# Kernel tuning notes

Hardware: AMD Instinct MI355X
Metric: run time of the kernel (lower is better)

Reference implementation:

```python
import jax, jax.numpy as jnp
import numpy as np

EPS = 1e-5      # InstanceNorm2d default eps
SLOPE = 0.2     # leaky relu negative_slope
K = 16          # neighbors
C = 128         # feature_dim


def _knn_idx(coords, k):
    # coords: [B,3,N] -> idx [B,N,k] of k nearest neighbors (excluding self)
    x = jnp.transpose(coords, (0, 2, 1))            # [B,N,3]
    sq = jnp.sum(x * x, axis=-1)                    # [B,N]
    dist = sq[:, :, None] + sq[:, None, :] - 2.0 * jnp.einsum('bnd,bmd->bnm', x, x)
    _, idx = jax.lax.top_k(-dist, k + 1)            # smallest distances, sorted
    return idx[:, :, 1:]                            # drop self


def _graph_feature(feats, idx):
    # feats: [B,C,N], idx: [B,N,k] -> [B,2C,N,k] = cat(center, neighbor-center)
    neigh = jax.vmap(lambda f, i: f[:, i])(feats, idx)   # [B,C,N,k]
    center = feats[:, :, :, None]
    return jnp.concatenate(
        [jnp.broadcast_to(center, neigh.shape), neigh - center], axis=1)


def _inorm(x):
    # InstanceNorm2d (affine=False): normalize each (b,c) over spatial dims
    mean = jnp.mean(x, axis=(2, 3), keepdims=True)
    var = jnp.mean((x - mean) ** 2, axis=(2, 3), keepdims=True)
    return (x - mean) * jax.lax.rsqrt(var + EPS)


def _edge_block(x, W):
    # 1x1 conv (W: [O,I]) + instance norm + leaky relu, x: [B,I,N,k]
    h = jnp.einsum('oi,bink->bonk', W, x)
    return jax.nn.leaky_relu(_inorm(h), SLOPE)


def setup_inputs() -> dict:
    key = jax.random.key(0)
    k1, k2, k3, k4, k5 = jax.random.split(key, 5)
    B, N = 2, 8192
    coords = jax.random.normal(k1, (B, 3, N), dtype=jnp.float32)
    features = jax.random.normal(k2, (B, C, N), dtype=jnp.float32)
    W1 = jax.random.normal(k3, (C, 2 * C), dtype=jnp.float32) * 0.05
    W2 = jax.random.normal(k4, (2 * C, 2 * C), dtype=jnp.float32) * 0.05
    W3 = jax.random.normal(k5, (C, 4 * C), dtype=jnp.float32) * 0.05
    return {"coords": coords, "features": features, "W1": W1, "W2": W2, "W3": W3}


def reference(coords, features, W1, W2, W3):
    idx = _knn_idx(coords, K)                       # [B,N,K]
    x0 = features                                   # [B,C,N]
    # block 1: EdgeConv C -> C
    x1 = _edge_block(_graph_feature(x0, idx), W1)   # [B,C,N,K]
    x1 = jnp.max(x1, axis=-1)                       # [B,C,N]
    # block 2: EdgeConv C -> 2C (same coords => same knn indices)
    x2 = _edge_block(_graph_feature(x1, idx), W2)   # [B,2C,N,K]
    x2 = jnp.max(x2, axis=-1)                       # [B,2C,N]
    # fuse: 1x1 conv 4C -> C + instance norm (over N) + leaky relu
    x3 = jnp.concatenate([x0, x1, x2], axis=1)      # [B,4C,N]
    h = jnp.einsum('oi,bin->bon', W3, x3)           # [B,C,N]
    h = _inorm(h[:, :, :, None])[:, :, :, 0]
    return jax.nn.leaky_relu(h, SLOPE)
```

## Files before the change

kernel.cpp:

```cpp
#include <hip/hip_runtime.h>
#include <hip/hip_bf16.h>
#include <cstdint>
#include <cstddef>

#define B_ 2
#define N_ 8192
#define C_ 128
#define K_ 16
#define NK_ (N_ * K_)
#define EPS_ 1e-5f
#define SLOPE_ 0.2f
#define INF_ 3.0e38f

typedef __attribute__((ext_vector_type(8))) short short8;
typedef __attribute__((ext_vector_type(4))) float f32x4;

static constexpr size_t OFF_IDX   = 0x000000;
static constexpr size_t OFF_CPK   = 0x100000;
static constexpr size_t OFF_CPK64 = 0x140000;
static constexpr size_t OFF_ACC   = 0x1C0000;
static constexpr size_t OFF_WC1   = 0x1D0000;
static constexpr size_t OFF_WC2   = 0x1E0000;
static constexpr size_t OFF_WB3   = 0x200000;
static constexpr size_t OFF_X3T   = 0x240000;
static constexpr size_t OFF_PQ    = OFF_X3T + (size_t)B_ * N_ * 512 * 2;

__device__ __forceinline__ __hip_bfloat16 ftob(float f) { return __float2bfloat16(f); }

__global__ void prep_kernel(const float* __restrict__ coords,
                            const float* __restrict__ W1,
                            const float* __restrict__ W2,
                            const float* __restrict__ W3,
                            __hip_bfloat16* __restrict__ wc1, __hip_bfloat16* __restrict__ wc2,
                            __hip_bfloat16* __restrict__ wb3,
                            float4* __restrict__ cpk, double4* __restrict__ cpk64,
                            float* __restrict__ acc) {
  int tid = blockIdx.x * 256 + threadIdx.x;
  if (tid < 32768) {
    int o = tid >> 7, i = tid & 127;
    float v;
    if (o < 128) v = W1[o * 256 + i] - W1[o * 256 + 128 + i];
    else         v = W1[(o - 128) * 256 + 128 + i];
    wc1[tid] = ftob(v);
  } else if (tid < 32768 + 65536) {
    int t2 = tid - 32768;
    int o = t2 >> 7, i = t2 & 127;
    float v;
    if (o < 256) v = W2[o * 256 + i] - W2[o * 256 + 128 + i];
    else         v = W2[(o - 256) * 256 + 128 + i];
    wc2[t2] = ftob(v);
  } else if (tid < 98304 + 65536) {
    int t2 = tid - 98304;
    wb3[t2] = ftob(W3[t2]);
  } else if (tid < 163840 + B_ * N_) {
    int q = tid - 163840;
    int b = q >> 13, n = q & (N_ - 1);
    float x = coords[(b * 3 + 0) * N_ + n];
    float y = coords[(b * 3 + 1) * N_ + n];
    float z = coords[(b * 3 + 2) * N_ + n];
    float sq = __fadd_rn(__fadd_rn(__fmul_rn(x, x), __fmul_rn(y, y)), __fmul_rn(z, z));
    cpk[q] = make_float4(x, y, z, sq);
    double xd = (double)x, yd = (double)y, zd = (double)z;
    double sqd = (xd * xd + yd * yd) + zd * zd;
    cpk64[q] = make_double4(xd, yd, zd, sqd);
  } else if (tid < 180224 + 2048) {
    acc[tid - 180224] = 0.f;
  }
}

__global__ __launch_bounds__(256) void transpose_kernel(const float* __restrict__ x0,
                                                        __hip_bfloat16* __restrict__ x3t) {
  __shared__ float tile[64 * 68];
  int b = blockIdx.z, c0 = blockIdx.y * 64, n0 = blockIdx.x * 64;
  int t = threadIdx.x;
  int r = t >> 4;
  int c4 = (t & 15) * 4;
#pragma unroll
  for (int i = 0; i < 4; ++i) {
    int row = r + i * 16;
    float4 v = *(const float4*)&x0[((size_t)(b * C_ + c0 + row)) * N_ + n0 + c4];
    *(float4*)&tile[row * 68 + c4] = v;
  }
  __syncthreads();
#pragma unroll
  for (int i = 0; i < 4; ++i) {
    int nl = r + i * 16;
    __hip_bfloat16* dst = &x3t[((size_t)(b * N_ + n0 + nl)) * 512 + c0 + c4];
    dst[0] = ftob(tile[(c4 + 0) * 68 + nl]);
    dst[1] = ftob(tile[(c4 + 1) * 68 + nl]);
    dst[2] = ftob(tile[(c4 + 2) * 68 + nl]);
    dst[3] = ftob(tile[(c4 + 3) * 68 + nl]);
  }
}

__device__ __forceinline__ float thresh17(float v, int lane) {
#pragma unroll
  for (int k2 = 2; k2 <= 64; k2 <<= 1) {
#pragma unroll
    for (int j = k2 >> 1; j > 0; j >>= 1) {
      float o = __shfl_xor(v, j, 64);
      bool up = ((lane & k2) == 0);
      bool lower = ((lane & j) == 0);
      v = ((lower == up)) ? fminf(v, o) : fmaxf(v, o);
    }
  }
  return __shfl(v, 16, 64);
}

__device__ __forceinline__ void bsort64d(double& d, int& ix, int lane) {
#pragma unroll
  for (int k2 = 2; k2 <= 64; k2 <<= 1) {
#pragma unroll
    for (int j = k2 >> 1; j > 0; j >>= 1) {
      double od = __shfl_xor(d, j, 64);
      int oi = __shfl_xor(ix, j, 64);
      bool up = ((lane & k2) == 0);
      bool lower = ((lane & j) == 0);
      bool takeMin = (lower == up);
      bool less = (od < d) || (od == d && oi < ix);
      if (takeMin == less) { d = od; ix = oi; }
    }
  }
}

__global__ __launch_bounds__(256) void knn_kernel(const float4* __restrict__ cpk,
                                                  const double4* __restrict__ cpk64,
                                                  int* __restrict__ idxout) {
  __shared__ int scnt[4][4];
  __shared__ int sii[4][4][128];
  int lane = threadIdx.x & 63;
  int wv = threadIdx.x >> 6;
  int q0 = (blockIdx.x * 4 + wv) * 4;
  int b = q0 >> 13;
  const float4* cb = cpk + (size_t)b * N_;
  const double4* cb64 = cpk64 + (size_t)b * N_;
  float4 me0 = cpk[q0], me1 = cpk[q0 + 1], me2 = cpk[q0 + 2], me3 = cpk[q0 + 3];

  if (lane < 4) scnt[wv][lane] = 0;
  __syncthreads();

  float m0 = INF_, m1 = INF_, m2 = INF_, m3 = INF_;
  for (int i = 0; i < 128; ++i) {
    float4 c = cb[i * 64 + lane];
    float d0 = fmaf(me0.z, c.z, fmaf(me0.y, c.y, me0.x * c.x));
    float d1 = fmaf(me1.z, c.z, fmaf(me1.y, c.y, me1.x * c.x));
    float d2 = fmaf(me2.z, c.z, fmaf(me2.y, c.y, me2.x * c.x));
    float d3 = fmaf(me3.z, c.z, fmaf(me3.y, c.y, me3.x * c.x));
    m0 = fminf(m0, fmaf(-2.0f, d0, c.w));
    m1 = fminf(m1, fmaf(-2.0f, d1, c.w));
    m2 = fminf(m2, fmaf(-2.0f, d2, c.w));
    m3 = fminf(m3, fmaf(-2.0f, d3, c.w));
  }
  float T0 = thresh17(m0, lane) + 1e-3f;
  float T1 = thresh17(m1, lane) + 1e-3f;
  float T2 = thresh17(m2, lane) + 1e-3f;
  float T3 = thresh17(m3, lane) + 1e-3f;

  for (int i = 0; i < 128; ++i) {
    float4 c = cb[i * 64 + lane];
    float d0 = fmaf(me0.z, c.z, fmaf(me0.y, c.y, me0.x * c.x));
    float d1 = fmaf(me1.z, c.z, fmaf(me1.y, c.y, me1.x * c.x));
    float d2 = fmaf(me2.z, c.z, fmaf(me2.y, c.y, me2.x * c.x));
    float d3 = fmaf(me3.z, c.z, fmaf(me3.y, c.y, me3.x * c.x));
    int m = i * 64 + lane;
    if (fmaf(-2.0f, d0, c.w) <= T0) { int p = atomicAdd(&scnt[wv][0], 1); if (p < 128) sii[wv][0][p] = m; }
    if (fmaf(-2.0f, d1, c.w) <= T1) { int p = atomicAdd(&scnt[wv][1], 1); if (p < 128) sii[wv][1][p] = m; }
    if (fmaf(-2.0f, d2, c.w) <= T2) { int p = atomicAdd(&scnt[wv][2], 1); if (p < 128) sii[wv][2][p] = m; }
    if (fmaf(-2.0f, d3, c.w) <= T3) { int p = atomicAdd(&scnt[wv][3], 1); if (p < 128) sii[wv][3][p] = m; }
  }
  __syncthreads();

#pragma unroll 1
  for (int j = 0; j < 4; ++j) {
    int q = q0 + j;
    int n = q & (N_ - 1);
    int cnt = scnt[wv][j] < 128 ? scnt[wv][j] : 128;
    double4 me64 = cb64[n];
    double d1 = 1e300; int ix1 = 0x7FFFFFFF;
    if (lane < cnt) {
      int m = sii[wv][j][lane];
      if (m != n) {
        double4 c = cb64[m];
        double dot = (me64.x * c.x + me64.y * c.y) + me64.z * c.z;
        d1 = (me64.w + c.w) - 2.0 * dot;
        ix1 = m;
      }
    }
    bsort64d(d1, ix1, lane);
    if (cnt > 64) {
      double d2 = 1e300; int ix2 = 0x7FFFFFFF;
      if (lane + 64 < cnt) {
        int m = sii[wv][j][lane + 64];
        if (m != n) {
          double4 c = cb64[m];
          double dot = (me64.x * c.x + me64.y * c.y) + me64.z * c.z;
          d2 = (me64.w + c.w) - 2.0 * dot;
          ix2 = m;
        }
      }
      bsort64d(d2, ix2, lane);
      int src = (lane - 16) & 63;
      double dB = __shfl(d2, src, 64);
      int iB = __shfl(ix2, src, 64);
      double nd = (lane < 16) ? d1 : ((lane < 32) ? dB : 1e300);
      int nix = (lane < 16) ? ix1 : ((lane < 32) ? iB : 0x7FFFFFFF);
      bsort64d(nd, nix, lane);
      d1 = nd; ix1 = nix;
    }
    if (lane < 16) idxout[(size_t)q * 16 + lane] = ix1;
  }
}

__global__ __launch_bounds__(256) void gemm_mfma(const __hip_bfloat16* __restrict__ X, int ldx,
                                                 const __hip_bfloat16* __restrict__ W, int ldw,
                                                 float* __restrict__ Cc, int ldc, int Ktot) {
  __shared__ short As[64 * 40];
  int b = blockIdx.z;
  int n0 = blockIdx.x * 64, o0 = blockIdx.y * 64;
  int t = threadIdx.x;
  int lane = t & 63, wv = t >> 6;
  int nh = (wv & 1) * 32, oh = (wv >> 1) * 32;
  const __hip_bfloat16* Xb = X + (size_t)(b * N_ + n0) * ldx;
  f32x4 acc00 = {0.f, 0.f, 0.f, 0.f}, acc01 = acc00, acc10 = acc00, acc11 = acc00;
  int sr = t >> 2;
  int sc = (t & 3) * 8;
  int arow = lane & 15;
  int kq = (lane >> 4) * 8;
  for (int kt = 0; kt < Ktot; kt += 32) {
    short8 av = *(const short8*)&Xb[(size_t)sr * ldx + kt + sc];
    *(short8*)&As[sr * 40 + sc] = av;
    __syncthreads();
    short8 a0 = *(const short8*)&As[(nh + arow) * 40 + kq];
    short8 a1 = *(const short8*)&As[(nh + 16 + arow) * 40 + kq];
    const __hip_bfloat16* Wp = W + (size_t)(o0 + oh + arow) * ldw + kt + kq;
    short8 b0 = *(const short8*)&Wp[0];
    short8 b1 = *(const short8*)&Wp[16 * (size_t)ldw];
    acc00 = __builtin_amdgcn_mfma_f32_16x16x32_bf16(a0, b0, acc00, 0, 0, 0);
    acc01 = __builtin_amdgcn_mfma_f32_16x16x32_bf16(a0, b1, acc01, 0, 0, 0);
    acc10 = __builtin_amdgcn_mfma_f32_16x16x32_bf16(a1, b0, acc10, 0, 0, 0);
    acc11 = __builtin_amdgcn_mfma_f32_16x16x32_bf16(a1, b1, acc11, 0, 0, 0);
    __syncthreads();
  }
  int crow = (lane >> 4) * 4;
  int ccol = lane & 15;
#pragma unroll
  for (int r = 0; r < 4; ++r) {
    size_t row0 = (size_t)(b * N_ + n0 + nh + crow + r) * ldc + o0 + oh;
    size_t row1 = (size_t)(b * N_ + n0 + nh + 16 + crow + r) * ldc + o0 + oh;
    Cc[row0 + ccol]      = acc00[r];
    Cc[row0 + 16 + ccol] = acc01[r];
    Cc[row1 + ccol]      = acc10[r];
    Cc[row1 + 16 + ccol] = acc11[r];
  }
}

template <int CO>
__global__ __launch_bounds__(256) void edge_kernel(const float* __restrict__ PQ,
                                                   const int* __restrict__ idx,
                                                   __hip_bfloat16* __restrict__ Mout,
                                                   float* __restrict__ acc) {
  constexpr int NG = 256 / CO;
  __shared__ float r1[256], r2[256];
  int b = blockIdx.y;
  int n0 = blockIdx.x * 64;
  int t = threadIdx.x;
  int o = t & (CO - 1);
  int qg = t / CO;
  float s1 = 0.f, s2 = 0.f;
  const float* PQb = PQ + (size_t)b * N_ * (2 * CO);
  for (int qq = qg; qq < 64; qq += NG) {
    int n = n0 + qq;
    const int4* ip = (const int4*)&idx[(size_t)(b * N_ + n) * 16];
    int4 i0 = ip[0], i1 = ip[1], i2 = ip[2], i3 = ip[3];
    float p = PQb[(size_t)n * (2 * CO) + o];
    float hmax = -INF_;
#define EDGE_STEP(mm)                                                    \
    { int mc = (mm) & (N_ - 1);                                          \
      float vv = PQb[(size_t)mc * (2 * CO) + CO + o];                    \
      float h = p + vv;                                                  \
      hmax = fmaxf(hmax, h); s1 += h; s2 = fmaf(h, h, s2); }
    EDGE_STEP(i0.x) EDGE_STEP(i0.y) EDGE_STEP(i0.z) EDGE_STEP(i0.w)
    EDGE_STEP(i1.x) EDGE_STEP(i1.y) EDGE_STEP(i1.z) EDGE_STEP(i1.w)
    EDGE_STEP(i2.x) EDGE_STEP(i2.y) EDGE_STEP(i2.z) EDGE_STEP(i2.w)
    EDGE_STEP(i3.x) EDGE_STEP(i3.y) EDGE_STEP(i3.z) EDGE_STEP(i3.w)
#undef EDGE_STEP
    Mout[(size_t)(b * N_ + n) * 512 + o] = ftob(hmax);
  }
  r1[t] = s1; r2[t] = s2;
  __syncthreads();
  if (t < CO) {
#pragma unroll
    for (int g = 1; g < NG; ++g) { s1 += r1[t + g * CO]; s2 += r2[t + g * CO]; }
    atomicAdd(&acc[(b * CO + o) * 2 + 0], s1);
    atomicAdd(&acc[(b * CO + o) * 2 + 1], s2);
  }
}

template <int CO>
__global__ void norm_kernel(__hip_bfloat16* __restrict__ M, const float* __restrict__ acc) {
  int tid = blockIdx.x * 256 + threadIdx.x;
  int o = tid & (CO - 1);
  int bn = tid / CO;
  int b = bn >> 13;
  float s1 = acc[(b * CO + o) * 2], s2 = acc[(b * CO + o) * 2 + 1];
  const float inv = 1.f / (float)NK_;
  float mean = s1 * inv;
  float var = fmaf(s2, inv, -mean * mean);
  float rs = rsqrtf(var + EPS_);
  float v = __bfloat162float(M[(size_t)bn * 512 + o]);
  float y = (v - mean) * rs;
  M[(size_t)bn * 512 + o] = ftob(y > 0.f ? y : SLOPE_ * y);
}

__global__ __launch_bounds__(256) void colred_kernel(const float* __restrict__ H,
                                                     float* __restrict__ acc3) {
  __shared__ float r1[256], r2[256];
  int b = blockIdx.y;
  int n0 = blockIdx.x * 256;
  int t = threadIdx.x;
  int o = t & 127, half = t >> 7;
  float s1 = 0.f, s2 = 0.f;
  for (int i = 0; i < 128; ++i) {
    int n = n0 + half * 128 + i;
    float v = H[(size_t)(b * N_ + n) * 128 + o];
    s1 += v; s2 = fmaf(v, v, s2);
  }
  r1[t] = s1; r2[t] = s2;
  __syncthreads();
  if (t < 128) {
    s1 = r1[t] + r1[t + 128];
    s2 = r2[t] + r2[t + 128];
    atomicAdd(&acc3[(b * 128 + o) * 2 + 0], s1);
    atomicAdd(&acc3[(b * 128 + o) * 2 + 1], s2);
  }
}

__global__ __launch_bounds__(256) void final_kernel(const float* __restrict__ H,
                                                    const float* __restrict__ acc3,
                                                    float* __restrict__ out) {
  __shared__ float tile[64 * 132];
  int b = blockIdx.y, n0 = blockIdx.x * 64;
  int t = threadIdx.x;
  int r = t >> 5;
  int c4 = (t & 31) * 4;
#pragma unroll
  for (int i = 0; i < 8; ++i) {
    int row = r + i * 8;
    *(float4*)&tile[row * 132 + c4] = *(const float4*)&H[(size_t)(b * N_ + n0 + row) * 128 + c4];
  }
  __syncthreads();
  int o = t >> 1;
  int nh = (t & 1) * 32;
  float s1 = acc3[(b * 128 + o) * 2], s2 = acc3[(b * 128 + o) * 2 + 1];
  const float inv = 1.f / (float)N_;
  float mean = s1 * inv;
  float var = fmaf(s2, inv, -mean * mean);
  float rs = rsqrtf(var + EPS_);
#pragma unroll
  for (int i = 0; i < 32; ++i) {
    int nl = nh + i;
    float v = tile[nl * 132 + o];
    float y = (v - mean) * rs;
    y = y > 0.f ? y : SLOPE_ * y;
    out[(size_t)(b * 128 + o) * N_ + n0 + nl] = y;
  }
}

extern "C" void kernel_launch(void* const* d_in, const int* in_sizes, int n_in,
                              void* d_out, int out_size, void* d_ws, size_t ws_size,
                              hipStream_t stream) {
  const float* coords = (const float*)d_in[0];
  const float* feats = (const float*)d_in[1];
  const float* W1 = (const float*)d_in[2];
  const float* W2 = (const float*)d_in[3];
  const float* W3 = (const float*)d_in[4];
  char* ws = (char*)d_ws;
  int* idx = (int*)(ws + OFF_IDX);
  float4* cpk = (float4*)(ws + OFF_CPK);
  double4* cpk64 = (double4*)(ws + OFF_CPK64);
  float* acc = (float*)(ws + OFF_ACC);
  __hip_bfloat16* wc1 = (__hip_bfloat16*)(ws + OFF_WC1);
  __hip_bfloat16* wc2 = (__hip_bfloat16*)(ws + OFF_WC2);
  __hip_bfloat16* wb3 = (__hip_bfloat16*)(ws + OFF_WB3);
  __hip_bfloat16* x3t = (__hip_bfloat16*)(ws + OFF_X3T);
  float* pq = (float*)(ws + OFF_PQ);

  prep_kernel<<<712, 256, 0, stream>>>(coords, W1, W2, W3, wc1, wc2, wb3, cpk, cpk64, acc);
  transpose_kernel<<<dim3(128, 2, 2), 256, 0, stream>>>(feats, x3t);
  knn_kernel<<<1024, 256, 0, stream>>>(cpk, cpk64, idx);
  gemm_mfma<<<dim3(128, 4, 2), 256, 0, stream>>>(x3t, 512, wc1, 128, pq, 256, 128);
  edge_kernel<128><<<dim3(128, 2), 256, 0, stream>>>(pq, idx, x3t + 128, acc + 0);
  norm_kernel<128><<<(B_ * N_ * 128) / 256, 256, 0, stream>>>(x3t + 128, acc + 0);
  gemm_mfma<<<dim3(128, 8, 2), 256, 0, stream>>>(x3t + 128, 512, wc2, 128, pq, 512, 128);
  edge_kernel<256><<<dim3(128, 2), 256, 0, stream>>>(pq, idx, x3t + 256, acc + 512);
  norm_kernel<256><<<(B_ * N_ * 256) / 256, 256, 0, stream>>>(x3t + 256, acc + 512);
  gemm_mfma<<<dim3(128, 2, 2), 256, 0, stream>>>(x3t, 512, wb3, 512, pq, 128, 512);
  colred_kernel<<<dim3(32, 2), 256, 0, stream>>>(pq, acc + 1536);
  final_kernel<<<dim3(128, 2), 256, 0, stream>>>(pq, acc + 1536, (float*)d_out);
}
```

Baseline: 226.8 us.

## Store edge-conv GEMM outputs in bf16 and process two channels per thread

The P/Q projection GEMMs for the two EdgeConv blocks now write bf16 instead of fp32. The edge gather kernel reads packed bf16 pairs, so each thread handles two channels with 32-bit loads, roughly halving gather traffic. The knn kernel also folds the -2 factor into precomputed coefficients and skips the atomic-insert path when no query hits. Rounding P and Q to bf16 adds error to the pre-norm activations and the instance-norm statistics.

After: 211.2 us. 6.9% less time.

```diff
diff --git a/kernel.cpp b/kernel.cpp
--- a/kernel.cpp
+++ b/kernel.cpp
@@ -26,6 +26,10 @@
 static constexpr size_t OFF_PQ    = OFF_X3T + (size_t)B_ * N_ * 512 * 2;
 
 __device__ __forceinline__ __hip_bfloat16 ftob(float f) { return __float2bfloat16(f); }
+__device__ __forceinline__ float bf2f(unsigned short h) {
+  unsigned u = ((unsigned)h) << 16;
+  return __uint_as_float(u);
+}
 
 __global__ void prep_kernel(const float* __restrict__ coords,
                             const float* __restrict__ W1,
@@ -135,6 +139,10 @@
   const float4* cb = cpk + (size_t)b * N_;
   const double4* cb64 = cpk64 + (size_t)b * N_;
   float4 me0 = cpk[q0], me1 = cpk[q0 + 1], me2 = cpk[q0 + 2], me3 = cpk[q0 + 3];
+  float a0x = -2.f * me0.x, a0y = -2.f * me0.y, a0z = -2.f * me0.z;
+  float a1x = -2.f * me1.x, a1y = -2.f * me1.y, a1z = -2.f * me1.z;
+  float a2x = -2.f * me2.x, a2y = -2.f * me2.y, a2z = -2.f * me2.z;
+  float a3x = -2.f * me3.x, a3y = -2.f * me3.y, a3z = -2.f * me3.z;
 
   if (lane < 4) scnt[wv][lane] = 0;
   __syncthreads();
@@ -142,14 +150,10 @@
   float m0 = INF_, m1 = INF_, m2 = INF_, m3 = INF_;
   for (int i = 0; i < 128; ++i) {
     float4 c = cb[i * 64 + lane];
-    float d0 = fmaf(me0.z, c.z, fmaf(me0.y, c.y, me0.x * c.x));
-    float d1 = fmaf(me1.z, c.z, fmaf(me1.y, c.y, me1.x * c.x));
-    float d2 = fmaf(me2.z, c.z, fmaf(me2.y, c.y, me2.x * c.x));
-    float d3 = fmaf(me3.z, c.z, fmaf(me3.y, c.y, me3.x * c.x));
-    m0 = fminf(m0, fmaf(-2.0f, d0, c.w));
-    m1 = fminf(m1, fmaf(-2.0f, d1, c.w));
-    m2 = fminf(m2, fmaf(-2.0f, d2, c.w));
-    m3 = fminf(m3, fmaf(-2.0f, d3, c.w));
+    m0 = fminf(m0, fmaf(a0z, c.z, fmaf(a0y, c.y, fmaf(a0x, c.x, c.w))));
+    m1 = fminf(m1, fmaf(a1z, c.z, fmaf(a1y, c.y, fmaf(a1x, c.x, c.w))));
+    m2 = fminf(m2, fmaf(a2z, c.z, fmaf(a2y, c.y, fmaf(a2x, c.x, c.w))));
+    m3 = fminf(m3, fmaf(a3z, c.z, fmaf(a3y, c.y, fmaf(a3x, c.x, c.w))));
   }
   float T0 = thresh17(m0, lane) + 1e-3f;
   float T1 = thresh17(m1, lane) + 1e-3f;
@@ -158,15 +162,18 @@
 
   for (int i = 0; i < 128; ++i) {
     float4 c = cb[i * 64 + lane];
-    float d0 = fmaf(me0.z, c.z, fmaf(me0.y, c.y, me0.x * c.x));
-    float d1 = fmaf(me1.z, c.z, fmaf(me1.y, c.y, me1.x * c.x));
-    float d2 = fmaf(me2.z, c.z, fmaf(me2.y, c.y, me2.x * c.x));
-    float d3 = fmaf(me3.z, c.z, fmaf(me3.y, c.y, me3.x * c.x));
-    int m = i * 64 + lane;
-    if (fmaf(-2.0f, d0, c.w) <= T0) { int p = atomicAdd(&scnt[wv][0], 1); if (p < 128) sii[wv][0][p] = m; }
-    if (fmaf(-2.0f, d1, c.w) <= T1) { int p = atomicAdd(&scnt[wv][1], 1); if (p < 128) sii[wv][1][p] = m; }
-    if (fmaf(-2.0f, d2, c.w) <= T2) { int p = atomicAdd(&scnt[wv][2], 1); if (p < 128) sii[wv][2][p] = m; }
-    if (fmaf(-2.0f, d3, c.w) <= T3) { int p = atomicAdd(&scnt[wv][3], 1); if (p < 128) sii[wv][3][p] = m; }
+    float p0 = fmaf(a0z, c.z, fmaf(a0y, c.y, fmaf(a0x, c.x, c.w)));
+    float p1 = fmaf(a1z, c.z, fmaf(a1y, c.y, fmaf(a1x, c.x, c.w)));
+    float p2 = fmaf(a2z, c.z, fmaf(a2y, c.y, fmaf(a2x, c.x, c.w)));
+    float p3 = fmaf(a3z, c.z, fmaf(a3y, c.y, fmaf(a3x, c.x, c.w)));
+    bool h0 = p0 <= T0, h1 = p1 <= T1, h2 = p2 <= T2, h3 = p3 <= T3;
+    if (h0 | h1 | h2 | h3) {
+      int m = i * 64 + lane;
+      if (h0) { int p = atomicAdd(&scnt[wv][0], 1); if (p < 128) sii[wv][0][p] = m; }
+      if (h1) { int p = atomicAdd(&scnt[wv][1], 1); if (p < 128) sii[wv][1][p] = m; }
+      if (h2) { int p = atomicAdd(&scnt[wv][2], 1); if (p < 128) sii[wv][2][p] = m; }
+      if (h3) { int p = atomicAdd(&scnt[wv][3], 1); if (p < 128) sii[wv][3][p] = m; }
+    }
   }
   __syncthreads();
 
@@ -211,9 +218,10 @@
   }
 }
 
+template <typename OUT>
 __global__ __launch_bounds__(256) void gemm_mfma(const __hip_bfloat16* __restrict__ X, int ldx,
                                                  const __hip_bfloat16* __restrict__ W, int ldw,
-                                                 float* __restrict__ Cc, int ldc, int Ktot) {
+                                                 OUT* __restrict__ Cc, int ldc, int Ktot) {
   __shared__ short As[64 * 40];
   int b = blockIdx.z;
   int n0 = blockIdx.x * 64, o0 = blockIdx.y * 64;
@@ -247,52 +255,72 @@
   for (int r = 0; r < 4; ++r) {
     size_t row0 = (size_t)(b * N_ + n0 + nh + crow + r) * ldc + o0 + oh;
     size_t row1 = (size_t)(b * N_ + n0 + nh + 16 + crow + r) * ldc + o0 + oh;
-    Cc[row0 + ccol]      = acc00[r];
-    Cc[row0 + 16 + ccol] = acc01[r];
-    Cc[row1 + ccol]      = acc10[r];
-    Cc[row1 + 16 + ccol] = acc11[r];
+    if constexpr (sizeof(OUT) == 4) {
+      Cc[row0 + ccol]      = acc00[r];
+      Cc[row0 + 16 + ccol] = acc01[r];
+      Cc[row1 + ccol]      = acc10[r];
+      Cc[row1 + 16 + ccol] = acc11[r];
+    } else {
+      Cc[row0 + ccol]      = ftob(acc00[r]);
+      Cc[row0 + 16 + ccol] = ftob(acc01[r]);
+      Cc[row1 + ccol]      = ftob(acc10[r]);
+      Cc[row1 + 16 + ccol] = ftob(acc11[r]);
+    }
   }
 }
 
 template <int CO>
-__global__ __launch_bounds__(256) void edge_kernel(const float* __restrict__ PQ,
+__global__ __launch_bounds__(256) void edge_kernel(const __hip_bfloat16* __restrict__ PQ,
                                                    const int* __restrict__ idx,
                                                    __hip_bfloat16* __restrict__ Mout,
                                                    float* __restrict__ acc) {
-  constexpr int NG = 256 / CO;
-  __shared__ float r1[256], r2[256];
+  constexpr int CP = CO / 2;
+  constexpr int NG = 256 / CP;
+  __shared__ float r1a[256], r1b[256], r2a[256], r2b[256];
   int b = blockIdx.y;
   int n0 = blockIdx.x * 64;
   int t = threadIdx.x;
-  int o = t & (CO - 1);
-  int qg = t / CO;
-  float s1 = 0.f, s2 = 0.f;
-  const float* PQb = PQ + (size_t)b * N_ * (2 * CO);
+  int oc = t & (CP - 1);
+  int o2 = oc * 2;
+  int qg = t / CP;
+  float s1a = 0.f, s1b = 0.f, s2a = 0.f, s2b = 0.f;
+  const __hip_bfloat16* PQb = PQ + (size_t)b * N_ * (2 * CO);
   for (int qq = qg; qq < 64; qq += NG) {
     int n = n0 + qq;
     const int4* ip = (const int4*)&idx[(size_t)(b * N_ + n) * 16];
     int4 i0 = ip[0], i1 = ip[1], i2 = ip[2], i3 = ip[3];
-    float p = PQb[(size_t)n * (2 * CO) + o];
-    float hmax = -INF_;
-#define EDGE_STEP(mm)                                                    \
-    { int mc = (mm) & (N_ - 1);                                          \
-      float vv = PQb[(size_t)mc * (2 * CO) + CO + o];                    \
-      float h = p + vv;                                                  \
-      hmax = fmaxf(hmax, h); s1 += h; s2 = fmaf(h, h, s2); }
+    unsigned pu = *(const unsigned*)&PQb[(size_t)n * (2 * CO) + o2];
+    float pa = bf2f((unsigned short)(pu & 0xFFFF));
+    float pb = bf2f((unsigned short)(pu >> 16));
+    float hma = -INF_, hmb = -INF_;
+#define EDGE_STEP(mm)                                                         \
+    { int mc = (mm) & (N_ - 1);                                               \
+      unsigned vu = *(const unsigned*)&PQb[(size_t)mc * (2 * CO) + CO + o2];  \
+      float ha = pa + bf2f((unsigned short)(vu & 0xFFFF));                    \
+      float hb = pb + bf2f((unsigned short)(vu >> 16));                       \
+      hma = fmaxf(hma, ha); s1a += ha; s2a = fmaf(ha, ha, s2a);               \
+      hmb = fmaxf(hmb, hb); s1b += hb; s2b = fmaf(hb, hb, s2b); }
     EDGE_STEP(i0.x) EDGE_STEP(i0.y) EDGE_STEP(i0.z) EDGE_STEP(i0.w)
     EDGE_STEP(i1.x) EDGE_STEP(i1.y) EDGE_STEP(i1.z) EDGE_STEP(i1.w)
     EDGE_STEP(i2.x) EDGE_STEP(i2.y) EDGE_STEP(i2.z) EDGE_STEP(i2.w)
     EDGE_STEP(i3.x) EDGE_STEP(i3.y) EDGE_STEP(i3.z) EDGE_STEP(i3.w)
 #undef EDGE_STEP
-    Mout[(size_t)(b * N_ + n) * 512 + o] = ftob(hmax);
-  }
-  r1[t] = s1; r2[t] = s2;
-  __syncthreads();
-  if (t < CO) {
-#pragma unroll
-    for (int g = 1; g < NG; ++g) { s1 += r1[t + g * CO]; s2 += r2[t + g * CO]; }
-    atomicAdd(&acc[(b * CO + o) * 2 + 0], s1);
-    atomicAdd(&acc[(b * CO + o) * 2 + 1], s2);
+    __hip_bfloat162 hh;
+    hh.x = ftob(hma); hh.y = ftob(hmb);
+    *(__hip_bfloat162*)&Mout[(size_t)(b * N_ + n) * 512 + o2] = hh;
+  }
+  r1a[t] = s1a; r1b[t] = s1b; r2a[t] = s2a; r2b[t] = s2b;
+  __syncthreads();
+  if (t < CP) {
+#pragma unroll
+    for (int g = 1; g < NG; ++g) {
+      s1a += r1a[t + g * CP]; s1b += r1b[t + g * CP];
+      s2a += r2a[t + g * CP]; s2b += r2b[t + g * CP];
+    }
+    atomicAdd(&acc[(b * CO + o2) * 2 + 0], s1a);
+    atomicAdd(&acc[(b * CO + o2) * 2 + 1], s2a);
+    atomicAdd(&acc[(b * CO + o2 + 1) * 2 + 0], s1b);
+    atomicAdd(&acc[(b * CO + o2 + 1) * 2 + 1], s2b);
   }
 }
 
@@ -383,18 +411,19 @@
   __hip_bfloat16* wc2 = (__hip_bfloat16*)(ws + OFF_WC2);
   __hip_bfloat16* wb3 = (__hip_bfloat16*)(ws + OFF_WB3);
   __hip_bfloat16* x3t = (__hip_bfloat16*)(ws + OFF_X3T);
-  float* pq = (float*)(ws + OFF_PQ);
+  __hip_bfloat16* pqb = (__hip_bfloat16*)(ws + OFF_PQ);
+  float* ht = (float*)(ws + OFF_PQ);
 
   prep_kernel<<<712, 256, 0, stream>>>(coords, W1, W2, W3, wc1, wc2, wb3, cpk, cpk64, acc);
   transpose_kernel<<<dim3(128, 2, 2), 256, 0, stream>>>(feats, x3t);
   knn_kernel<<<1024, 256, 0, stream>>>(cpk, cpk64, idx);
-  gemm_mfma<<<dim3(128, 4, 2), 256, 0, stream>>>(x3t, 512, wc1, 128, pq, 256, 128);
-  edge_kernel<128><<<dim3(128, 2), 256, 0, stream>>>(pq, idx, x3t + 128, acc + 0);
+  gemm_mfma<__hip_bfloat16><<<dim3(128, 4, 2), 256, 0, stream>>>(x3t, 512, wc1, 128, pqb, 256, 128);
+  edge_kernel<128><<<dim3(128, 2), 256, 0, stream>>>(pqb, idx, x3t + 128, acc + 0);
   norm_kernel<128><<<(B_ * N_ * 128) / 256, 256, 0, stream>>>(x3t + 128, acc + 0);
-  gemm_mfma<<<dim3(128, 8, 2), 256, 0, stream>>>(x3t + 128, 512, wc2, 128, pq, 512, 128);
-  edge_kernel<256><<<dim3(128, 2), 256, 0, stream>>>(pq, idx, x3t + 256, acc + 512);
+  gemm_mfma<__hip_bfloat16><<<dim3(128, 8, 2), 256, 0, stream>>>(x3t + 128, 512, wc2, 128, pqb, 512, 128);
+  edge_kernel<256><<<dim3(128, 2), 256, 0, stream>>>(pqb, idx, x3t + 256, acc + 512);
   norm_kernel<256><<<(B_ * N_ * 256) / 256, 256, 0, stream>>>(x3t + 256, acc + 512);
-  gemm_mfma<<<dim3(128, 2, 2), 256, 0, stream>>>(x3t, 512, wb3, 512, pq, 128, 512);
-  colred_kernel<<<dim3(32, 2), 256, 0, stream>>>(pq, acc + 1536);
-  final_kernel<<<dim3(128, 2), 256, 0, stream>>>(pq, acc + 1536, (float*)d_out);
-}
+  gemm_mfma<float><<<dim3(128, 2, 2), 256, 0, stream>>>(x3t, 512, wb3, 512, ht, 128, 512);
+  colred_kernel<<<dim3(32, 2), 256, 0, stream>>>(ht, acc + 1536);
+  final_kernel<<<dim3(128, 2), 256, 0, stream>>>(ht, acc + 1536, (float*)d_out);
+}
```
